# Optimization experiments

Hardware: AMD Instinct MI355X
Metric: run time of the kernel (lower is better)

The kernel has to match this reference:

```python
import jax, jax.numpy as jnp
import numpy as np

PAD_ID = 0
B, T, V, E, H = 64, 128, 10000, 300, 1024


def _lstm_step(x, h, c, w_ih, w_hh, b):
    # standard LSTM cell: gates = x@W_ih + h@W_hh + b, split into i,f,g,o
    gates = x @ w_ih + h @ w_hh + b  # [B, 4H]
    i, f, g, o = jnp.split(gates, 4, axis=-1)
    c2 = jax.nn.sigmoid(f) * c + jax.nn.sigmoid(i) * jnp.tanh(g)
    h2 = jax.nn.sigmoid(o) * jnp.tanh(c2)
    return h2, c2


def setup_inputs() -> dict:
    key = jax.random.key(0)
    ks = jax.random.split(key, 12)
    sent = jax.random.randint(ks[0], (B, T), 0, V)
    length = jax.random.randint(ks[1], (B,), 1, T)
    sc_e, sc_h = 1.0 / np.sqrt(E), 1.0 / np.sqrt(H)
    wordvec = jax.random.normal(ks[2], (V, E), jnp.float32) * 0.1
    w_ih0 = jax.random.normal(ks[3], (E, 4 * H), jnp.float32) * sc_e
    w_hh0 = jax.random.normal(ks[4], (H, 4 * H), jnp.float32) * sc_h
    b0 = jnp.zeros((4 * H,), jnp.float32)
    w_ih1 = jax.random.normal(ks[5], (H, 4 * H), jnp.float32) * sc_h
    w_hh1 = jax.random.normal(ks[6], (H, 4 * H), jnp.float32) * sc_h
    b1 = jnp.zeros((4 * H,), jnp.float32)
    w_out = jax.random.normal(ks[7], (H, V), jnp.float32) * sc_h
    b_out = jnp.zeros((V,), jnp.float32)
    return {"sent": sent, "length": length, "wordvec": wordvec,
            "w_ih0": w_ih0, "w_hh0": w_hh0, "b0": b0,
            "w_ih1": w_ih1, "w_hh1": w_hh1, "b1": b1,
            "w_out": w_out, "b_out": b_out}


def reference(sent, length, wordvec, w_ih0, w_hh0, b0, w_ih1, w_hh1, b1, w_out, b_out):
    # torch.tensor(self.wordvec[sent]) detaches the embedding -> stop_gradient
    emb = jax.lax.stop_gradient(wordvec[sent])          # [B, T, E]
    xs = jnp.swapaxes(emb[:, :-1], 0, 1)                # [T-1, B, E]
    zeros = jnp.zeros((sent.shape[0], w_hh0.shape[0]), emb.dtype)
    init = ((zeros, zeros), (zeros, zeros))             # (h,c) per layer

    def step(carry, x):
        (h0, c0), (h1, c1) = carry
        h0, c0 = _lstm_step(x, h0, c0, w_ih0, w_hh0, b0)
        h1, c1 = _lstm_step(h0, h1, c1, w_ih1, w_hh1, b1)
        logits = h1 @ w_out + b_out                     # [B, V]
        return ((h0, c0), (h1, c1)), logits

    _, logits = jax.lax.scan(step, init, xs)            # [T-1, B, V]
    temp = jnp.swapaxes(logits, 0, 1)                   # [B, T-1, V]
    gt = sent[:, 1:]                                    # [B, T-1]
    # log(softmax(logits)).gather(gt) == log_softmax gathered (same math, stable)
    logp = jnp.take_along_axis(jax.nn.log_softmax(temp, axis=-1), gt[..., None], axis=-1)[..., 0]
    logp = jnp.where(gt == PAD_ID, 0.0, logp)
    per_sent = -jnp.sum(logp, axis=1) / length.astype(temp.dtype)
    loss = jnp.sum(per_sent)
    return loss, temp
```

## Files before the change

kernel.cpp:

```cpp
#include <hip/hip_runtime.h>
#include <hip/hip_bf16.h>
#include <math.h>

#define BB 64
#define TT 128
#define VV 10000
#define EE 300
#define HH 1024
#define TM1 127

typedef __hip_bfloat16 bf16;
typedef __attribute__((ext_vector_type(8))) short s8v;
typedef __attribute__((ext_vector_type(4))) float f4v;

__global__ void zero_kernel(float* __restrict__ p, int n) {
    int i = blockIdx.x * blockDim.x + threadIdx.x;
    if (i < n) p[i] = 0.0f;
}

__global__ void embed_kernel(const int* __restrict__ sent,
                             const float* __restrict__ wordvec,
                             bf16* __restrict__ X) {
    int bi = blockIdx.x;
    int t = bi >> 6;
    int b = bi & 63;
    int w = (t < TM1) ? sent[b * TT + t] : 0;
    const float* src = wordvec + (long)w * EE;
    bf16* dst = X + (long)bi * 320;
    for (int e = threadIdx.x; e < 320; e += 64) {
        float v = (t < TM1 && e < EE) ? src[e] : 0.0f;
        dst[e] = __float2bfloat16(v);
    }
}

__global__ void transpose_bf16_kernel(const float* __restrict__ src,
                                      bf16* __restrict__ dst,
                                      int K, int N, int Kpad) {
    __shared__ float tile[32][33];
    int n0 = blockIdx.x * 32, k0 = blockIdx.y * 32;
    int tid = threadIdx.x;
    {
        int tn = tid & 31, tk = tid >> 5;
        #pragma unroll
        for (int i = 0; i < 4; i++) {
            int k = tk + i * 8;
            float v = (k0 + k < K && n0 + tn < N) ? src[(long)(k0 + k) * N + n0 + tn] : 0.0f;
            tile[k][tn] = v;
        }
    }
    __syncthreads();
    {
        int wk = tid & 31, wn = tid >> 5;
        #pragma unroll
        for (int i = 0; i < 4; i++) {
            int n = wn + i * 8;
            dst[(long)(n0 + n) * Kpad + k0 + wk] = __float2bfloat16(tile[wk][n]);
        }
    }
}

__global__ __launch_bounds__(256) void step_kernel(
    const bf16* __restrict__ X, int ta, int tb, int a_only,
    const bf16* __restrict__ h0_in, bf16* __restrict__ h0_out,
    const bf16* __restrict__ h1_in, bf16* __restrict__ h1_out,
    const bf16* __restrict__ wt_ih0, const bf16* __restrict__ wt_hh0,
    const bf16* __restrict__ wt_ih1, const bf16* __restrict__ wt_hh1,
    const float* __restrict__ b0, const float* __restrict__ b1,
    float* __restrict__ c0, float* __restrict__ c1,
    bf16* __restrict__ H1)
{
    __shared__ float gbuf[4][16][17];
    int bid = blockIdx.x;
    int isA, pb;
    if (a_only) { isA = 1; pb = bid; }
    else        { isA = (bid >= 256); pb = bid & 255; }
    const int j = pb & 63, r = pb >> 6;
    const int tid = threadIdx.x;
    const int g = tid >> 6, L = tid & 63, quad = L >> 4, l16 = L & 15;

    const int arow = r * 16 + l16;
    const int wrow = g * HH + j * 16 + l16;

    f4v acc0 = {0.f, 0.f, 0.f, 0.f};
    f4v acc1 = {0.f, 0.f, 0.f, 0.f};

    if (isA) {
        const s8v* ax = (const s8v*)(X + ((long)(ta * 64 + arow)) * 320 + quad * 8);
        const s8v* bx = (const s8v*)(wt_ih0 + (long)wrow * 320 + quad * 8);
        #pragma unroll
        for (int k = 0; k < 10; k++) {
            if (k & 1) acc1 = __builtin_amdgcn_mfma_f32_16x16x32_bf16(ax[k*4], bx[k*4], acc1, 0, 0, 0);
            else       acc0 = __builtin_amdgcn_mfma_f32_16x16x32_bf16(ax[k*4], bx[k*4], acc0, 0, 0, 0);
        }
        const s8v* ah = (const s8v*)(h0_in + (long)arow * HH + quad * 8);
        const s8v* bh = (const s8v*)(wt_hh0 + (long)wrow * HH + quad * 8);
        #pragma unroll
        for (int k = 0; k < 32; k++) {
            if (k & 1) acc1 = __builtin_amdgcn_mfma_f32_16x16x32_bf16(ah[k*4], bh[k*4], acc1, 0, 0, 0);
            else       acc0 = __builtin_amdgcn_mfma_f32_16x16x32_bf16(ah[k*4], bh[k*4], acc0, 0, 0, 0);
        }
    } else {
        const s8v* a0 = (const s8v*)(h0_in + (long)arow * HH + quad * 8);
        const s8v* b0f = (const s8v*)(wt_ih1 + (long)wrow * HH + quad * 8);
        #pragma unroll
        for (int k = 0; k < 32; k++) {
            if (k & 1) acc1 = __builtin_amdgcn_mfma_f32_16x16x32_bf16(a0[k*4], b0f[k*4], acc1, 0, 0, 0);
            else       acc0 = __builtin_amdgcn_mfma_f32_16x16x32_bf16(a0[k*4], b0f[k*4], acc0, 0, 0, 0);
        }
        const s8v* a1 = (const s8v*)(h1_in + (long)arow * HH + quad * 8);
        const s8v* b1f = (const s8v*)(wt_hh1 + (long)wrow * HH + quad * 8);
        #pragma unroll
        for (int k = 0; k < 32; k++) {
            if (k & 1) acc1 = __builtin_amdgcn_mfma_f32_16x16x32_bf16(a1[k*4], b1f[k*4], acc1, 0, 0, 0);
            else       acc0 = __builtin_amdgcn_mfma_f32_16x16x32_bf16(a1[k*4], b1f[k*4], acc0, 0, 0, 0);
        }
    }
    acc0 += acc1;

    #pragma unroll
    for (int i = 0; i < 4; i++) gbuf[g][quad * 4 + i][l16] = acc0[i];
    __syncthreads();

    {
        int row = tid >> 4, col = tid & 15;
        int hrow = r * 16 + row, hcol = j * 16 + col;
        const float* bias = isA ? b0 : b1;
        float gi = gbuf[0][row][col] + bias[hcol];
        float gf = gbuf[1][row][col] + bias[HH + hcol];
        float gg = gbuf[2][row][col] + bias[2 * HH + hcol];
        float go = gbuf[3][row][col] + bias[3 * HH + hcol];
        float* cst = isA ? c0 : c1;
        int idx = hrow * HH + hcol;
        float c = cst[idx];
        float si = 1.0f / (1.0f + expf(-gi));
        float sf = 1.0f / (1.0f + expf(-gf));
        float so = 1.0f / (1.0f + expf(-go));
        float cn = sf * c + si * tanhf(gg);
        float hn = so * tanhf(cn);
        cst[idx] = cn;
        bf16 hb = __float2bfloat16(hn);
        if (isA) h0_out[idx] = hb;
        else {
            h1_out[idx] = hb;
            H1[((long)hrow * TM1 + tb) * HH + hcol] = hb;
        }
    }
}

__global__ __launch_bounds__(256) void out_gemm_mfma(
    const bf16* __restrict__ A, const bf16* __restrict__ Wt,
    const float* __restrict__ bias, float* __restrict__ out)
{
    int tid = threadIdx.x, w = tid >> 6, L = tid & 63, quad = L >> 4, l16 = L & 15;
    int wr = w >> 1, wc = w & 1;
    long R0 = (long)blockIdx.y * 128 + wr * 64;
    long C0 = (long)blockIdx.x * 128 + wc * 64;

    f4v acc[4][4] = {};
    const s8v* ap[4];
    const s8v* bp[4];
    #pragma unroll
    for (int i = 0; i < 4; i++) ap[i] = (const s8v*)(A + (R0 + i * 16 + l16) * 1024 + quad * 8);
    #pragma unroll
    for (int jj = 0; jj < 4; jj++) bp[jj] = (const s8v*)(Wt + (C0 + jj * 16 + l16) * 1024 + quad * 8);

    for (int k = 0; k < 32; k++) {
        s8v av[4], bv[4];
        #pragma unroll
        for (int i = 0; i < 4; i++) av[i] = ap[i][k * 4];
        #pragma unroll
        for (int jj = 0; jj < 4; jj++) bv[jj] = bp[jj][k * 4];
        #pragma unroll
        for (int i = 0; i < 4; i++)
            #pragma unroll
            for (int jj = 0; jj < 4; jj++)
                acc[i][jj] = __builtin_amdgcn_mfma_f32_16x16x32_bf16(av[i], bv[jj], acc[i][jj], 0, 0, 0);
    }

    #pragma unroll
    for (int i = 0; i < 4; i++) {
        #pragma unroll
        for (int jj = 0; jj < 4; jj++) {
            #pragma unroll
            for (int p = 0; p < 4; p++) {
                long row = R0 + i * 16 + quad * 4 + p;
                long col = C0 + jj * 16 + l16;
                if (row < 8128 && col < VV)
                    out[row * VV + col] = acc[i][jj][p] + bias[col];
            }
        }
    }
}

__global__ __launch_bounds__(256) void loss_kernel(
    const float* __restrict__ logits,
    const int* __restrict__ sent,
    float* __restrict__ rowloss)
{
    __shared__ float red[256];
    int r = blockIdx.x;
    int b = r / TM1, t = r % TM1;
    const float* row = logits + (long)r * VV;
    int tid = threadIdx.x;

    float mx = -INFINITY;
    for (int v = tid; v < VV; v += 256) mx = fmaxf(mx, row[v]);
    red[tid] = mx; __syncthreads();
    for (int s = 128; s > 0; s >>= 1) {
        if (tid < s) red[tid] = fmaxf(red[tid], red[tid + s]);
        __syncthreads();
    }
    mx = red[0];
    __syncthreads();

    float sum = 0.0f;
    for (int v = tid; v < VV; v += 256) sum += expf(row[v] - mx);
    red[tid] = sum; __syncthreads();
    for (int s = 128; s > 0; s >>= 1) {
        if (tid < s) red[tid] += red[tid + s];
        __syncthreads();
    }
    if (tid == 0) {
        int gt = sent[b * TT + t + 1];
        float val = 0.0f;
        if (gt != 0) val = -(row[gt] - mx - logf(red[0]));
        rowloss[r] = val;
    }
}

__global__ void final_kernel(const float* __restrict__ rowloss,
                             const int* __restrict__ length,
                             float* __restrict__ out0)
{
    int b = threadIdx.x;
    float s = 0.0f;
    for (int t = 0; t < TM1; t++) s += rowloss[b * TM1 + t];
    s /= (float)length[b];
    #pragma unroll
    for (int off = 32; off > 0; off >>= 1) s += __shfl_down(s, off, 64);
    if (b == 0) out0[0] = s;
}

extern "C" void kernel_launch(void* const* d_in, const int* in_sizes, int n_in,
                              void* d_out, int out_size, void* d_ws, size_t ws_size,
                              hipStream_t stream) {
    const int*   sent    = (const int*)d_in[0];
    const int*   length  = (const int*)d_in[1];
    const float* wordvec = (const float*)d_in[2];
    const float* w_ih0   = (const float*)d_in[3];
    const float* w_hh0   = (const float*)d_in[4];
    const float* b0      = (const float*)d_in[5];
    const float* w_ih1   = (const float*)d_in[6];
    const float* w_hh1   = (const float*)d_in[7];
    const float* b1      = (const float*)d_in[8];
    const float* w_out   = (const float*)d_in[9];
    const float* b_out   = (const float*)d_in[10];
    float* out = (float*)d_out;

    char* W = (char*)d_ws;
    size_t o = 0;
    bf16* X      = (bf16*)(W + o); o += 128L * 64 * 320 * 2;
    bf16* wtih0  = (bf16*)(W + o); o += 4096L * 320 * 2;
    bf16* wthh0  = (bf16*)(W + o); o += 4096L * 1024 * 2;
    bf16* wtih1  = (bf16*)(W + o); o += 4096L * 1024 * 2;
    bf16* wthh1  = (bf16*)(W + o); o += 4096L * 1024 * 2;
    bf16* woutt  = (bf16*)(W + o); o += 10112L * 1024 * 2;
    bf16* H1     = (bf16*)(W + o); o += 8192L * 1024 * 2;
    bf16*  h0b0  = (bf16*)(W + o); o += 64L * 1024 * 2;
    bf16*  h1b0  = (bf16*)(W + o); o += 64L * 1024 * 2;
    float* c0    = (float*)(W + o); o += 64L * 1024 * 4;
    float* c1    = (float*)(W + o); o += 64L * 1024 * 4;
    bf16*  h0b1  = (bf16*)(W + o); o += 64L * 1024 * 2;
    bf16*  h1b1  = (bf16*)(W + o); o += 64L * 1024 * 2;
    float* rowloss = (float*)(W + o); o += 8128L * 4;

    zero_kernel<<<768, 256, 0, stream>>>((float*)h0b0, 196608);
    embed_kernel<<<128 * 64, 64, 0, stream>>>(sent, wordvec, X);
    transpose_bf16_kernel<<<dim3(128, 10), 256, 0, stream>>>(w_ih0, wtih0, 300, 4096, 320);
    transpose_bf16_kernel<<<dim3(128, 32), 256, 0, stream>>>(w_hh0, wthh0, 1024, 4096, 1024);
    transpose_bf16_kernel<<<dim3(128, 32), 256, 0, stream>>>(w_ih1, wtih1, 1024, 4096, 1024);
    transpose_bf16_kernel<<<dim3(128, 32), 256, 0, stream>>>(w_hh1, wthh1, 1024, 4096, 1024);
    transpose_bf16_kernel<<<dim3(316, 32), 256, 0, stream>>>(w_out, woutt, 1024, VV, 1024);

    step_kernel<<<256, 256, 0, stream>>>(
        X, 0, 0, 1,
        h0b0, h0b1, h1b0, h1b1,
        wtih0, wthh0, wtih1, wthh1, b0, b1, c0, c1, H1);

    for (int t = 0; t < TM1; t++) {
        bf16* h0in  = (t & 1) ? h0b0 : h0b1;
        bf16* h0out = (t & 1) ? h0b1 : h0b0;
        bf16* h1in  = (t & 1) ? h1b1 : h1b0;
        bf16* h1out = (t & 1) ? h1b0 : h1b1;
        step_kernel<<<512, 256, 0, stream>>>(
            X, t + 1, t, 0,
            h0in, h0out, h1in, h1out,
            wtih0, wthh0, wtih1, wthh1, b0, b1, c0, c1, H1);
    }

    out_gemm_mfma<<<dim3(79, 64), 256, 0, stream>>>(H1, woutt, b_out, out + 1);
    loss_kernel<<<TM1 * BB, 256, 0, stream>>>(out + 1, sent, rowloss);
    final_kernel<<<1, 64, 0, stream>>>(rowloss, length, out);
}
```

Before: 4.587 ms.

## Widen LSTM step blocks to cover all batch rows; stage output GEMM tiles in LDS

The step kernel now launches 1024-thread blocks that each handle one 16-column hidden slice across all 64 batch rows, so each weight tile is fetched once per block rather than by four separate blocks. Inner loops are only partially unrolled. The output projection GEMM now stages 128x32 A and B tiles into shared memory with async global-to-LDS copies, so the four waves share loads instead of each reading global memory directly. The step kernel uses fewer, larger blocks (128 vs 512), which may reduce parallelism per step, and the GEMM adds two barriers per k-tile with no double buffering.

```diff
diff --git a/kernel.cpp b/kernel.cpp
--- a/kernel.cpp
+++ b/kernel.cpp
@@ -12,6 +12,11 @@
 typedef __hip_bfloat16 bf16;
 typedef __attribute__((ext_vector_type(8))) short s8v;
 typedef __attribute__((ext_vector_type(4))) float f4v;
+
+__device__ __forceinline__ void async_copy16(const void* g, void* s) {
+    __builtin_amdgcn_global_load_lds((const __attribute__((address_space(1))) void*)g,
+                                     (__attribute__((address_space(3))) void*)s, 16, 0, 0);
+}
 
 __global__ void zero_kernel(float* __restrict__ p, int n) {
     int i = blockIdx.x * blockDim.x + threadIdx.x;
@@ -59,7 +64,7 @@
     }
 }
 
-__global__ __launch_bounds__(256) void step_kernel(
+__global__ __launch_bounds__(1024) void step_kernel(
     const bf16* __restrict__ X, int ta, int tb, int a_only,
     const bf16* __restrict__ h0_in, bf16* __restrict__ h0_out,
     const bf16* __restrict__ h1_in, bf16* __restrict__ h1_out,
@@ -69,16 +74,16 @@
     float* __restrict__ c0, float* __restrict__ c1,
     bf16* __restrict__ H1)
 {
-    __shared__ float gbuf[4][16][17];
+    __shared__ float gbuf[4][64][17];
     int bid = blockIdx.x;
-    int isA, pb;
-    if (a_only) { isA = 1; pb = bid; }
-    else        { isA = (bid >= 256); pb = bid & 255; }
-    const int j = pb & 63, r = pb >> 6;
+    int isA, j;
+    if (a_only) { isA = 1; j = bid; }
+    else        { isA = (bid >= 64); j = bid & 63; }
     const int tid = threadIdx.x;
-    const int g = tid >> 6, L = tid & 63, quad = L >> 4, l16 = L & 15;
-
-    const int arow = r * 16 + l16;
+    const int wave = tid >> 6, g = wave & 3, m = wave >> 2;
+    const int L = tid & 63, quad = L >> 4, l16 = L & 15;
+
+    const int arow = m * 16 + l16;
     const int wrow = g * HH + j * 16 + l16;
 
     f4v acc0 = {0.f, 0.f, 0.f, 0.f};
@@ -94,7 +99,7 @@
         }
         const s8v* ah = (const s8v*)(h0_in + (long)arow * HH + quad * 8);
         const s8v* bh = (const s8v*)(wt_hh0 + (long)wrow * HH + quad * 8);
-        #pragma unroll
+        #pragma unroll 8
         for (int k = 0; k < 32; k++) {
             if (k & 1) acc1 = __builtin_amdgcn_mfma_f32_16x16x32_bf16(ah[k*4], bh[k*4], acc1, 0, 0, 0);
             else       acc0 = __builtin_amdgcn_mfma_f32_16x16x32_bf16(ah[k*4], bh[k*4], acc0, 0, 0, 0);
@@ -102,14 +107,14 @@
     } else {
         const s8v* a0 = (const s8v*)(h0_in + (long)arow * HH + quad * 8);
         const s8v* b0f = (const s8v*)(wt_ih1 + (long)wrow * HH + quad * 8);
-        #pragma unroll
+        #pragma unroll 8
         for (int k = 0; k < 32; k++) {
             if (k & 1) acc1 = __builtin_amdgcn_mfma_f32_16x16x32_bf16(a0[k*4], b0f[k*4], acc1, 0, 0, 0);
             else       acc0 = __builtin_amdgcn_mfma_f32_16x16x32_bf16(a0[k*4], b0f[k*4], acc0, 0, 0, 0);
         }
         const s8v* a1 = (const s8v*)(h1_in + (long)arow * HH + quad * 8);
         const s8v* b1f = (const s8v*)(wt_hh1 + (long)wrow * HH + quad * 8);
-        #pragma unroll
+        #pragma unroll 8
         for (int k = 0; k < 32; k++) {
             if (k & 1) acc1 = __builtin_amdgcn_mfma_f32_16x16x32_bf16(a1[k*4], b1f[k*4], acc1, 0, 0, 0);
             else       acc0 = __builtin_amdgcn_mfma_f32_16x16x32_bf16(a1[k*4], b1f[k*4], acc0, 0, 0, 0);
@@ -118,19 +123,19 @@
     acc0 += acc1;
 
     #pragma unroll
-    for (int i = 0; i < 4; i++) gbuf[g][quad * 4 + i][l16] = acc0[i];
+    for (int i = 0; i < 4; i++) gbuf[g][m * 16 + quad * 4 + i][l16] = acc0[i];
     __syncthreads();
 
     {
         int row = tid >> 4, col = tid & 15;
-        int hrow = r * 16 + row, hcol = j * 16 + col;
+        int hcol = j * 16 + col;
         const float* bias = isA ? b0 : b1;
         float gi = gbuf[0][row][col] + bias[hcol];
         float gf = gbuf[1][row][col] + bias[HH + hcol];
         float gg = gbuf[2][row][col] + bias[2 * HH + hcol];
         float go = gbuf[3][row][col] + bias[3 * HH + hcol];
         float* cst = isA ? c0 : c1;
-        int idx = hrow * HH + hcol;
+        int idx = row * HH + hcol;
         float c = cst[idx];
         float si = 1.0f / (1.0f + expf(-gi));
         float sf = 1.0f / (1.0f + expf(-gf));
@@ -142,7 +147,7 @@
         if (isA) h0_out[idx] = hb;
         else {
             h1_out[idx] = hb;
-            H1[((long)hrow * TM1 + tb) * HH + hcol] = hb;
+            H1[((long)row * TM1 + tb) * HH + hcol] = hb;
         }
     }
 }
@@ -151,30 +156,51 @@
     const bf16* __restrict__ A, const bf16* __restrict__ Wt,
     const float* __restrict__ bias, float* __restrict__ out)
 {
+    __shared__ __align__(16) bf16 As[128 * 32];
+    __shared__ __align__(16) bf16 Bs[128 * 32];
     int tid = threadIdx.x, w = tid >> 6, L = tid & 63, quad = L >> 4, l16 = L & 15;
     int wr = w >> 1, wc = w & 1;
-    long R0 = (long)blockIdx.y * 128 + wr * 64;
-    long C0 = (long)blockIdx.x * 128 + wc * 64;
+    long R0 = (long)blockIdx.y * 128;
+    long C0 = (long)blockIdx.x * 128;
+
+    int srow = tid >> 2;
+    int kcol = (tid & 3) * 8;
+    const bf16* gA0 = A  + (R0 + srow) * 1024 + kcol;
+    const bf16* gA1 = A  + (R0 + 64 + srow) * 1024 + kcol;
+    const bf16* gB0 = Wt + (C0 + srow) * 1024 + kcol;
+    const bf16* gB1 = Wt + (C0 + 64 + srow) * 1024 + kcol;
+    char* sA = (char*)As + w * 1024;
+    char* sB = (char*)Bs + w * 1024;
+
+    const s8v* fA[4];
+    const s8v* fB[4];
+    #pragma unroll
+    for (int i = 0; i < 4; i++) fA[i] = (const s8v*)&As[(wr * 64 + i * 16 + l16) * 32 + quad * 8];
+    #pragma unroll
+    for (int jj = 0; jj < 4; jj++) fB[jj] = (const s8v*)&Bs[(wc * 64 + jj * 16 + l16) * 32 + quad * 8];
 
     f4v acc[4][4] = {};
-    const s8v* ap[4];
-    const s8v* bp[4];
-    #pragma unroll
-    for (int i = 0; i < 4; i++) ap[i] = (const s8v*)(A + (R0 + i * 16 + l16) * 1024 + quad * 8);
-    #pragma unroll
-    for (int jj = 0; jj < 4; jj++) bp[jj] = (const s8v*)(Wt + (C0 + jj * 16 + l16) * 1024 + quad * 8);
-
-    for (int k = 0; k < 32; k++) {
+
+    for (int kt = 0; kt < 32; ++kt) {
+        async_copy16(gA0, sA);
+        async_copy16(gA1, sA + 4096);
+        async_copy16(gB0, sB);
+        async_copy16(gB1, sB + 4096);
+        gA0 += 32; gA1 += 32; gB0 += 32; gB1 += 32;
+        __syncthreads();
+
         s8v av[4], bv[4];
         #pragma unroll
-        for (int i = 0; i < 4; i++) av[i] = ap[i][k * 4];
-        #pragma unroll
-        for (int jj = 0; jj < 4; jj++) bv[jj] = bp[jj][k * 4];
+        for (int i = 0; i < 4; i++) av[i] = *fA[i];
+        #pragma unroll
+        for (int jj = 0; jj < 4; jj++) bv[jj] = *fB[jj];
         #pragma unroll
         for (int i = 0; i < 4; i++)
             #pragma unroll
             for (int jj = 0; jj < 4; jj++)
                 acc[i][jj] = __builtin_amdgcn_mfma_f32_16x16x32_bf16(av[i], bv[jj], acc[i][jj], 0, 0, 0);
+
+        __syncthreads();
     }
 
     #pragma unroll
@@ -183,8 +209,8 @@
         for (int jj = 0; jj < 4; jj++) {
             #pragma unroll
             for (int p = 0; p < 4; p++) {
-                long row = R0 + i * 16 + quad * 4 + p;
-                long col = C0 + jj * 16 + l16;
+                long row = R0 + wr * 64 + i * 16 + quad * 4 + p;
+                long col = C0 + wc * 64 + jj * 16 + l16;
                 if (row < 8128 && col < VV)
                     out[row * VV + col] = acc[i][jj][p] + bias[col];
             }
@@ -282,7 +308,7 @@
     transpose_bf16_kernel<<<dim3(128, 32), 256, 0, stream>>>(w_hh1, wthh1, 1024, 4096, 1024);
     transpose_bf16_kernel<<<dim3(316, 32), 256, 0, stream>>>(w_out, woutt, 1024, VV, 1024);
 
-    step_kernel<<<256, 256, 0, stream>>>(
+    step_kernel<<<64, 1024, 0, stream>>>(
         X, 0, 0, 1,
         h0b0, h0b1, h1b0, h1b1,
         wtih0, wthh0, wtih1, wthh1, b0, b1, c0, c1, H1);
@@ -292,7 +318,7 @@
         bf16* h0out = (t & 1) ? h0b1 : h0b0;
         bf16* h1in  = (t & 1) ? h1b1 : h1b0;
         bf16* h1out = (t & 1) ? h1b0 : h1b1;
-        step_kernel<<<512, 256, 0, stream>>>(
+        step_kernel<<<128, 1024, 0, stream>>>(
             X, t + 1, t, 0,
             h0in, h0out, h1in, h1out,
             wtih0, wthh0, wtih1, wthh1, b0, b1, c0, c1, H1);
```

New measurement: 8.436 ms. 83.9% more time.
